# Performance work log

Hardware: AMD Instinct MI355X
Metric: run time of the kernel (lower is better)

## Reference

```python
import jax, jax.numpy as jnp
import numpy as np

N = 20000       # nodes per graph
E = 320000      # edges per graph (avg degree 16)
R = 8           # num_relations
B = 2           # batch of graphs
DIMS = [128, 256, 256, 128]  # in -> hidden -> hidden -> out
SLOPE = 0.2     # LeakyReLU negative slope


def setup_inputs() -> dict:
    key = jax.random.key(0)
    ks = jax.random.split(key, 12)
    inp = {
        "x": jax.random.normal(ks[0], (B, N, DIMS[0]), dtype=jnp.float32),
        "edge_index": jax.random.randint(ks[1], (B, 2, E), 0, N, dtype=jnp.int32),
        "edge_type": jax.random.randint(ks[2], (B, E), 0, R, dtype=jnp.int32),
    }
    for l in range(3):
        cin, cout = DIMS[l], DIMS[l + 1]
        s = 1.0 / np.sqrt(cin)
        inp[f"W{l}"] = jax.random.normal(ks[3 + 3 * l], (R, cin, cout), jnp.float32) * s
        inp[f"root{l}"] = jax.random.normal(ks[4 + 3 * l], (cin, cout), jnp.float32) * s
        inp[f"b{l}"] = jnp.zeros((cout,), jnp.float32)
    return inp


def _rgcn_layer(h, src, dst, etype, W, root, b):
    """One RGCNConv (per-relation mean aggregation) on a single graph.
    h: (N,Cin), src/dst/etype: (E,), W: (R,Cin,Cout), root: (Cin,Cout), b: (Cout,)
    """
    # transform every node by every relation weight once: (N,R,Cout)
    h_rel = jnp.einsum('nc,rcd->nrd', h, W)
    # per-edge message: gather source node transformed by that edge's relation
    msg = h_rel[src, etype]                               # (E,Cout)
    # per-(target-node, relation) mean, as in PyG's per-relation propagate
    seg = dst * R + etype                                 # (E,)
    sums = jax.ops.segment_sum(msg, seg, num_segments=N * R)
    cnt = jax.ops.segment_sum(jnp.ones((msg.shape[0],), h.dtype), seg,
                              num_segments=N * R)
    mean = sums / jnp.maximum(cnt, 1.0)[:, None]          # (N*R,Cout)
    agg = mean.reshape(N, R, -1).sum(axis=1)              # (N,Cout)
    return agg + h @ root + b


def reference(x, edge_index, edge_type, W0, root0, b0, W1, root1, b1, W2, root2, b2):
    params = [(W0, root0, b0), (W1, root1, b1), (W2, root2, b2)]

    def single(xg, ei, et):
        src, dst = ei[0], ei[1]
        h = xg
        for (W, root, b) in params:
            h = _rgcn_layer(h, src, dst, et, W, root, b)
            h = jnp.where(h > 0, h, SLOPE * h)  # LeakyReLU(0.2); dropout=identity (eval)
        return h

    return jax.vmap(single)(x, edge_index, edge_type)
```

## Files before the change

### kernel.cpp

```cpp
#include <hip/hip_runtime.h>
#include <hip/hip_bf16.h>

#define NN 20000
#define EE 320000
#define RR 8
#define NR (NN * RR)
#define NB 40
#define SCAP 640

typedef float f32x4 __attribute__((ext_vector_type(4)));
typedef short s16x8 __attribute__((ext_vector_type(8)));

__device__ __forceinline__ unsigned short f2bf(float f) {
  unsigned u = __builtin_bit_cast(unsigned, f);
  unsigned r = u + 0x7FFFu + ((u >> 16) & 1u);
  return (unsigned short)(r >> 16);
}
__device__ __forceinline__ float bf2f(unsigned short u) {
  return __builtin_bit_cast(float, (unsigned)u << 16);
}
__device__ __forceinline__ void gload_lds16(const void* g, void* l) {
  __builtin_amdgcn_global_load_lds(
      (const __attribute__((address_space(1))) unsigned*)g,
      (__attribute__((address_space(3))) unsigned*)l, 16, 0, 0);
}

__global__ void k_count(const int* __restrict__ ei, const int* __restrict__ et,
                        int* __restrict__ cnt) {
  int e = blockIdx.x * blockDim.x + threadIdx.x;
  int g = e >= EE;
  int el = e - g * EE;
  int d = ei[(size_t)g * 2 * EE + EE + el];
  int t = et[(size_t)g * EE + el];
  atomicAdd(&cnt[(size_t)g * NR + d * RR + t], 1);
}

__global__ __launch_bounds__(1024) void k_scan1(const int* __restrict__ cnt,
                                                int* __restrict__ off,
                                                int* __restrict__ btot) {
  int g = blockIdx.y, b = blockIdx.x;
  const int* c = cnt + (size_t)g * NR;
  int* o = off + (size_t)g * NR;
  __shared__ int wsum[16];
  int lane = threadIdx.x & 63, w = threadIdx.x >> 6;
  int i = b * 4096 + (int)threadIdx.x * 4;
  int4 v = {0, 0, 0, 0};
  if (i + 3 < NR) v = *(const int4*)&c[i];
  else {
    if (i < NR) v.x = c[i];
    if (i + 1 < NR) v.y = c[i + 1];
    if (i + 2 < NR) v.z = c[i + 2];
  }
  int s0 = v.x, s1 = s0 + v.y, s2 = s1 + v.z, s3 = s2 + v.w;
  int s = s3;
  for (int d = 1; d < 64; d <<= 1) {
    int t = __shfl_up(s, d);
    if (lane >= d) s += t;
  }
  if (lane == 63) wsum[w] = s;
  __syncthreads();
  if (threadIdx.x < 16) {
    int ws = wsum[threadIdx.x];
    for (int d = 1; d < 16; d <<= 1) {
      int t = __shfl_up(ws, d);
      if ((int)threadIdx.x >= d) ws += t;
    }
    wsum[threadIdx.x] = ws;
  }
  __syncthreads();
  int excl = (w > 0 ? wsum[w - 1] : 0) + (s - s3);
  if (i < NR) o[i] = excl;
  if (i + 1 < NR) o[i + 1] = excl + s0;
  if (i + 2 < NR) o[i + 2] = excl + s1;
  if (i + 3 < NR) o[i + 3] = excl + s2;
  if (threadIdx.x == 0) btot[g * NB + b] = wsum[15];
}

__global__ void k_scan2(const int* __restrict__ btot, int* __restrict__ bof) {
  int g = threadIdx.x >> 6, lane = threadIdx.x & 63;
  int v = (lane < NB) ? btot[g * NB + lane] : 0;
  int s = v;
  for (int d = 1; d < 64; d <<= 1) {
    int t = __shfl_up(s, d);
    if (lane >= d) s += t;
  }
  if (lane < NB) bof[g * NB + lane] = s - v;
}

__global__ __launch_bounds__(1024) void k_scan3(int* __restrict__ off,
                                                const int* __restrict__ bof) {
  int g = blockIdx.y;
  int add = bof[g * NB + blockIdx.x];
  int i = blockIdx.x * 4096 + (int)threadIdx.x * 4;
  int* o = off + (size_t)g * NR;
  if (i + 3 < NR) {
    int4 v = *(const int4*)&o[i];
    v.x += add; v.y += add; v.z += add; v.w += add;
    *(int4*)&o[i] = v;
  } else {
    for (int j = i; j < NR; ++j) o[j] += add;
  }
}

__global__ void k_scatter(const int* __restrict__ ei, const int* __restrict__ et,
                          int* __restrict__ off, int* __restrict__ ssrc) {
  int e = blockIdx.x * blockDim.x + threadIdx.x;
  int g = e >= EE;
  int el = e - g * EE;
  int s = ei[(size_t)g * 2 * EE + el];
  int d = ei[(size_t)g * 2 * EE + EE + el];
  int t = et[(size_t)g * EE + el];
  int pos = atomicAdd(&off[(size_t)g * NR + d * RR + t], 1);
  ssrc[(size_t)g * EE + pos] = s;
}

__global__ void k_cvt(const float* __restrict__ x, unsigned short* __restrict__ hX) {
  int i = (blockIdx.x * blockDim.x + threadIdx.x) * 4;
  if (i >= 2 * NN * 128) return;
  int g = i >= NN * 128;
  int il = i - g * NN * 128;
  float4 v = *(const float4*)&x[i];
  ushort4 o;
  o.x = f2bf(v.x); o.y = f2bf(v.y); o.z = f2bf(v.z); o.w = f2bf(v.w);
  *(ushort4*)&hX[(size_t)g * NN * 256 + il] = o;
}

__global__ void k_btf(const float* __restrict__ W, const float* __restrict__ root,
                      unsigned short* __restrict__ btf, int Cin, int Cout,
                      int Ktot) {
  int idx = blockIdx.x * blockDim.x + threadIdx.x;
  if (idx >= Cout * Ktot) return;
  int j = idx & 7;
  int lane = (idx >> 3) & 63;
  int kk = (idx >> 9) & 1;
  int t = idx >> 10;
  int fr = t % (Cout / 16);
  int s = t / (Cout / 16);
  int co = fr * 16 + (lane & 15);
  int k = s * 64 + kk * 32 + (lane >> 4) * 8 + j;
  int r = k / Cin, ci = k - r * Cin;
  float v = (r < RR) ? W[((size_t)r * Cin + ci) * Cout + co]
                     : root[(size_t)ci * Cout + co];
  btf[idx] = f2bf(v);
}

#define LOADB(bb, s)                                                           \
  _Pragma("unroll") for (int kk = 0; kk < 2; ++kk)                             \
      _Pragma("unroll") for (int f = 0; f < 4; ++f) bb[kk][f] =                \
          *(const s16x8*)(btl +                                                \
                          (size_t)(((s) * (COUT / 16) + wn16 + f) * 2 + kk) *  \
                              512);

#define MFMA_STEP_C(Ab, c, bb)                                                 \
  do {                                                                         \
    _Pragma("unroll") for (int kk = 0; kk < 2; ++kk) {                         \
      s16x8 a[MF];                                                             \
      _Pragma("unroll") for (int f = 0; f < MF; ++f) {                         \
        int row = wm + f * 16 + (lane & 15);                                   \
        int colb = kk * 64 + (lane >> 4) * 16;                                 \
        a[f] = *(const s16x8*)((Ab) + (c)*ASTR + row * 128 +                   \
                               (colb ^ ((row & 7) << 4)));                     \
      }                                                                        \
      _Pragma("unroll") for (int fm = 0; fm < MF; ++fm)                        \
          _Pragma("unroll") for (int fn = 0; fn < 4; ++fn)                     \
              acc[fm][fn] = __builtin_amdgcn_mfma_f32_16x16x32_bf16(           \
                  a[fm], bb[kk][fn], acc[fm][fn], 0, 0, 0);                    \
    }                                                                          \
  } while (0)

#define ACC4(u)                                                                \
  {                                                                            \
    faH[c][0] += __builtin_bit_cast(float, (u).x & 0xFFFF0000u);               \
    faL[c][0] += __builtin_bit_cast(float, (u).x << 16);                       \
    faH[c][1] += __builtin_bit_cast(float, (u).y & 0xFFFF0000u);               \
    faL[c][1] += __builtin_bit_cast(float, (u).y << 16);                       \
    faH[c][2] += __builtin_bit_cast(float, (u).z & 0xFFFF0000u);               \
    faL[c][2] += __builtin_bit_cast(float, (u).z << 16);                       \
    faH[c][3] += __builtin_bit_cast(float, (u).w & 0xFFFF0000u);               \
    faL[c][3] += __builtin_bit_cast(float, (u).w << 16);                       \
  }

template <int CIN, int COUT, bool OUTF32>
__global__ __launch_bounds__(256) void k_fused(
    const int* __restrict__ ssrc, const int* __restrict__ off,
    const unsigned short* __restrict__ h, const unsigned short* __restrict__ btf,
    const float* __restrict__ bias, void* __restrict__ outp) {
  constexpr int KTOT = (RR + 1) * CIN;
  constexpr int NS = KTOT / 64;
  constexpr int CH = CIN / 64;
  constexpr int CPT = CIN / 8;
  constexpr int NCH = CPT / 8;
  constexpr int NWN = COUT / 64;
  constexpr int MW = 4 / NWN;
  constexpr int WR = 32 / MW;
  constexpr int MF = WR / 16;
  constexpr int ASTR = 4112;
  constexpr int SH = (CIN == 256) ? 9 : 8;
  __shared__ char As[2][CH * ASTR];
  __shared__ int offs[32][9];
  __shared__ int sseg[SCAP];
  const int tid = threadIdx.x, lane = tid & 63, wave = tid >> 6;
  const int wn = (wave % NWN) * 64;
  const int wn16 = wn >> 4;
  const int wm = (wave / NWN) * WR;
  const int m0 = blockIdx.x * 32;
  const int g = blockIdx.z;
  ssrc += (size_t)g * EE;
  off += (size_t)g * NR;
  h += (size_t)g * NN * 256;

  for (int idx = tid; idx < 32 * 9; idx += 256) {
    int row = idx / 9, j = idx - row * 9;
    int seg0 = (m0 + row) * RR;
    offs[row][j] = (j == 0) ? (seg0 == 0 ? 0 : off[seg0 - 1]) : off[seg0 + j - 1];
  }
  const int segA = m0 * RR;
  const int ebase = (segA == 0) ? 0 : off[segA - 1];
  const int eend = off[(m0 + 32) * RR - 1];
  const int cntE = eend - ebase;
  const bool inl = cntE <= SCAP;
  if (inl)
    for (int i = tid; i < cntE; i += 256) sseg[i] = ssrc[ebase + i] << SH;
  __syncthreads();

  f32x4 acc[MF][4] = {};
  const int arow = tid >> 3;
  const int q = tid & 7;
  const int swzA = (arow & 7) << 4;
  const char* hqB = (const char*)h + (size_t)q * CPT * 2;
  const unsigned short* btl = btf + lane * 8;

  auto produce = [&](int r, int buf) {
    float faL[NCH][4], faH[NCH][4];
#pragma unroll
    for (int c = 0; c < NCH; ++c)
#pragma unroll
      for (int w = 0; w < 4; ++w) { faL[c][w] = 0.f; faH[c][w] = 0.f; }
    const int o0 = offs[arow][r], o1 = offs[arow][r + 1];
    if (inl) {
      int e = o0 - ebase;
      const int e1 = o1 - ebase;
      for (; e + 1 < e1; e += 2) {
        const unsigned short* pa = (const unsigned short*)(hqB + sseg[e]);
        const unsigned short* pb = (const unsigned short*)(hqB + sseg[e + 1]);
#pragma unroll
        for (int c = 0; c < NCH; ++c) {
          uint4 ua = *(const uint4*)(pa + c * 8);
          uint4 ub = *(const uint4*)(pb + c * 8);
          ACC4(ua);
          ACC4(ub);
        }
      }
      if (e < e1) {
        const unsigned short* pa = (const unsigned short*)(hqB + sseg[e]);
#pragma unroll
        for (int c = 0; c < NCH; ++c) {
          uint4 ua = *(const uint4*)(pa + c * 8);
          ACC4(ua);
        }
      }
    } else {
      for (int e = o0; e < o1; ++e) {
        const unsigned short* pa = (const unsigned short*)(hqB + (ssrc[e] << SH));
#pragma unroll
        for (int c = 0; c < NCH; ++c) {
          uint4 ua = *(const uint4*)(pa + c * 8);
          ACC4(ua);
        }
      }
    }
    float inv = 1.0f / fmaxf((float)(o1 - o0), 1.0f);
#pragma unroll
    for (int c = 0; c < NCH; ++c) {
      s16x8 mbv;
#pragma unroll
      for (int w = 0; w < 4; ++w) {
        mbv[2 * w] = (short)f2bf(faL[c][w] * inv);
        mbv[2 * w + 1] = (short)f2bf(faH[c][w] * inv);
      }
      int colb = (q * CPT + c * 8) * 2;
      int ct = colb >> 7;
      int wb = colb & 127;
      *(s16x8*)(As[buf] + ct * ASTR + arow * 128 + (wb ^ swzA)) = mbv;
    }
  };

  auto root_stage = [&]() {
#pragma unroll
    for (int i = 0; i < CH; ++i) {
      int o = i * ASTR + wave * 1024;
      int ob = wave * 1024 + lane * 16;
      int row = (ob >> 7) & 31;
      int wb = ob & 127;
      gload_lds16((const char*)h + ((size_t)(m0 + row) * CIN + i * 64) * 2 +
                      (wb ^ ((row & 7) << 4)),
                  As[RR & 1] + o);
    }
  };

  s16x8 bc[2][4], bn[2][4];
  LOADB(bc, 0);
  produce(0, 0);
  __syncthreads();

  for (int r = 0; r <= RR; ++r) {
    const char* Ab = As[r & 1];
#pragma unroll
    for (int c = 0; c < CH; c += 2) {
      int s = r * CH + c;
      if (s + 1 < NS) { LOADB(bn, s + 1); }
      __builtin_amdgcn_s_setprio(1);
      MFMA_STEP_C(Ab, c, bc);
      __builtin_amdgcn_s_setprio(0);
      if (s + 2 < NS) { LOADB(bc, s + 2); }
      __builtin_amdgcn_s_setprio(1);
      MFMA_STEP_C(Ab, c + 1, bn);
      __builtin_amdgcn_s_setprio(0);
    }
    if (r + 1 < RR) produce(r + 1, (r + 1) & 1);
    else if (r + 1 == RR) root_stage();
    __syncthreads();
  }

#pragma unroll
  for (int fm = 0; fm < MF; ++fm) {
    int rbase = m0 + wm + fm * 16 + (lane >> 4) * 4;
#pragma unroll
    for (int fn = 0; fn < 4; ++fn) {
      int col = wn + fn * 16 + (lane & 15);
      float bv = bias[col];
#pragma unroll
      for (int v = 0; v < 4; ++v) {
        int row = rbase + v;
        float xv = acc[fm][fn][v] + bv;
        xv = xv > 0.f ? xv : 0.2f * xv;
        if constexpr (OUTF32)
          ((float*)outp)[(size_t)g * NN * COUT + (size_t)row * COUT + col] = xv;
        else
          ((unsigned short*)outp)[(size_t)g * NN * 256 + (size_t)row * COUT +
                                  col] = f2bf(xv);
      }
    }
  }
}

extern "C" void kernel_launch(void* const* d_in, const int* in_sizes, int n_in,
                              void* d_out, int out_size, void* d_ws, size_t ws_size,
                              hipStream_t stream) {
  const float* x  = (const float*)d_in[0];
  const int* ei   = (const int*)d_in[1];
  const int* etp  = (const int*)d_in[2];
  const float* W0 = (const float*)d_in[3];
  const float* r0 = (const float*)d_in[4];
  const float* b0 = (const float*)d_in[5];
  const float* W1 = (const float*)d_in[6];
  const float* r1 = (const float*)d_in[7];
  const float* b1 = (const float*)d_in[8];
  const float* W2 = (const float*)d_in[9];
  const float* r2 = (const float*)d_in[10];
  const float* b2 = (const float*)d_in[11];

  char* p = (char*)d_ws;
  unsigned short* hX  = (unsigned short*)p; p += (size_t)2 * NN * 256 * 2;
  unsigned short* h_a = (unsigned short*)p; p += (size_t)2 * NN * 256 * 2;
  int* cnt  = (int*)p; p += (size_t)2 * NR * 4;
  int* off  = (int*)p; p += (size_t)2 * NR * 4;
  int* btot = (int*)p; p += (size_t)2 * NB * 4;
  int* bof  = (int*)p; p += (size_t)2 * NB * 4;
  int* ssrc = (int*)p; p += (size_t)2 * EE * 4;
  unsigned short* bt0 = (unsigned short*)p; p += (size_t)256 * 1152 * 2;
  unsigned short* bt1 = (unsigned short*)p; p += (size_t)256 * 2304 * 2;
  unsigned short* bt2 = (unsigned short*)p; p += (size_t)128 * 2304 * 2;

  k_btf<<<(256 * 1152 + 255) / 256, 256, 0, stream>>>(W0, r0, bt0, 128, 256, 1152);
  k_btf<<<(256 * 2304 + 255) / 256, 256, 0, stream>>>(W1, r1, bt1, 256, 256, 2304);
  k_btf<<<(128 * 2304 + 255) / 256, 256, 0, stream>>>(W2, r2, bt2, 256, 128, 2304);

  (void)hipMemsetAsync(cnt, 0, (size_t)2 * NR * 4, stream);
  k_count<<<2 * EE / 256, 256, 0, stream>>>(ei, etp, cnt);
  k_scan1<<<dim3(NB, 2), 1024, 0, stream>>>(cnt, off, btot);
  k_scan2<<<1, 128, 0, stream>>>(btot, bof);
  k_scan3<<<dim3(NB, 2), 1024, 0, stream>>>(off, bof);
  k_cvt<<<2 * NN * 128 / 4 / 256, 256, 0, stream>>>(x, hX);
  k_scatter<<<2 * EE / 256, 256, 0, stream>>>(ei, etp, off, ssrc);

  k_fused<128, 256, false><<<dim3(625, 1, 2), 256, 0, stream>>>(
      ssrc, off, hX, bt0, b0, h_a);
  k_fused<256, 256, false><<<dim3(625, 1, 2), 256, 0, stream>>>(
      ssrc, off, h_a, bt1, b1, hX);
  k_fused<256, 128, true><<<dim3(625, 1, 2), 256, 0, stream>>>(
      ssrc, off, hX, bt2, b2, d_out);
}
```

Baseline: 364.4 us.

## Process two relations per phase to halve block barriers in fused RGCN kernel

Restructures the fused gather+GEMM loop so both LDS halves are filled with two relations' mean aggregates, then consumed together, with the root stage last. This replaces per-relation double-buffered overlap (produce next while MFMA on current) with a produce-both/compute-both scheme that uses two barriers per pair of relations. It cuts barrier count and loop overhead but removes the overlap of gather latency with MFMA work, since produce now runs between barriers rather than alongside compute.

```diff
diff --git a/kernel.cpp b/kernel.cpp
--- a/kernel.cpp
+++ b/kernel.cpp
@@ -151,14 +151,14 @@
                           (size_t)(((s) * (COUT / 16) + wn16 + f) * 2 + kk) *  \
                               512);
 
-#define MFMA_STEP_C(Ab, c, bb)                                                 \
+#define MFMA_STEP_C(c, bb)                                                     \
   do {                                                                         \
     _Pragma("unroll") for (int kk = 0; kk < 2; ++kk) {                         \
       s16x8 a[MF];                                                             \
       _Pragma("unroll") for (int f = 0; f < MF; ++f) {                         \
         int row = wm + f * 16 + (lane & 15);                                   \
         int colb = kk * 64 + (lane >> 4) * 16;                                 \
-        a[f] = *(const s16x8*)((Ab) + (c)*ASTR + row * 128 +                   \
+        a[f] = *(const s16x8*)(As + (c)*ASTR + row * 128 +                     \
                                (colb ^ ((row & 7) << 4)));                     \
       }                                                                        \
       _Pragma("unroll") for (int fm = 0; fm < MF; ++fm)                        \
@@ -196,7 +196,7 @@
   constexpr int MF = WR / 16;
   constexpr int ASTR = 4112;
   constexpr int SH = (CIN == 256) ? 9 : 8;
-  __shared__ char As[2][CH * ASTR];
+  __shared__ char As[2 * CH * ASTR];
   __shared__ int offs[32][9];
   __shared__ int sseg[SCAP];
   const int tid = threadIdx.x, lane = tid & 63, wave = tid >> 6;
@@ -230,7 +230,7 @@
   const char* hqB = (const char*)h + (size_t)q * CPT * 2;
   const unsigned short* btl = btf + lane * 8;
 
-  auto produce = [&](int r, int buf) {
+  auto produce = [&](int r) {
     float faL[NCH][4], faH[NCH][4];
 #pragma unroll
     for (int c = 0; c < NCH; ++c)
@@ -270,6 +270,7 @@
       }
     }
     float inv = 1.0f / fmaxf((float)(o1 - o0), 1.0f);
+    char* half = As + (r & 1) * (CH * ASTR);
 #pragma unroll
     for (int c = 0; c < NCH; ++c) {
       s16x8 mbv;
@@ -281,7 +282,7 @@
       int colb = (q * CPT + c * 8) * 2;
       int ct = colb >> 7;
       int wb = colb & 127;
-      *(s16x8*)(As[buf] + ct * ASTR + arow * 128 + (wb ^ swzA)) = mbv;
+      *(s16x8*)(half + ct * ASTR + arow * 128 + (wb ^ swzA)) = mbv;
     }
   };
 
@@ -294,32 +295,49 @@
       int wb = ob & 127;
       gload_lds16((const char*)h + ((size_t)(m0 + row) * CIN + i * 64) * 2 +
                       (wb ^ ((row & 7) << 4)),
-                  As[RR & 1] + o);
+                  As + o);
     }
   };
 
   s16x8 bc[2][4], bn[2][4];
   LOADB(bc, 0);
-  produce(0, 0);
+  produce(0);
+  produce(1);
   __syncthreads();
 
-  for (int r = 0; r <= RR; ++r) {
-    const char* Ab = As[r & 1];
-#pragma unroll
-    for (int c = 0; c < CH; c += 2) {
-      int s = r * CH + c;
-      if (s + 1 < NS) { LOADB(bn, s + 1); }
+  for (int p = 0; p < 4; ++p) {
+#pragma unroll
+    for (int c = 0; c < 2 * CH; c += 2) {
+      int s = p * 2 * CH + c;
+      LOADB(bn, s + 1);
       __builtin_amdgcn_s_setprio(1);
-      MFMA_STEP_C(Ab, c, bc);
+      MFMA_STEP_C(c, bc);
       __builtin_amdgcn_s_setprio(0);
       if (s + 2 < NS) { LOADB(bc, s + 2); }
       __builtin_amdgcn_s_setprio(1);
-      MFMA_STEP_C(Ab, c + 1, bn);
+      MFMA_STEP_C(c + 1, bn);
       __builtin_amdgcn_s_setprio(0);
     }
-    if (r + 1 < RR) produce(r + 1, (r + 1) & 1);
-    else if (r + 1 == RR) root_stage();
     __syncthreads();
+    if (p < 3) {
+      produce(2 * p + 2);
+      produce(2 * p + 3);
+    } else {
+      root_stage();
+    }
+    __syncthreads();
+  }
+#pragma unroll
+  for (int c = 0; c < CH; c += 2) {
+    int s = RR * CH + c;
+    if (s + 1 < NS) { LOADB(bn, s + 1); }
+    __builtin_amdgcn_s_setprio(1);
+    MFMA_STEP_C(c, bc);
+    __builtin_amdgcn_s_setprio(0);
+    if (s + 2 < NS) { LOADB(bc, s + 2); }
+    __builtin_amdgcn_s_setprio(1);
+    MFMA_STEP_C(c + 1, bn);
+    __builtin_amdgcn_s_setprio(0);
   }
 
 #pragma unroll
```

Measured after the change: 349.8 us. 1.04x faster.
